# Kernel tuning notes

Hardware: AMD Instinct MI355X
Metric: run time of the kernel (lower is better)

Reference implementation:

```python
import jax, jax.numpy as jnp
import numpy as np

N = 20000      # nodes
E = 320000     # edges
F = 32         # node_feat_dim
H = 128        # hidden_dim
HEADS = 4
DH = 128       # out_channels per head (PyG TransformerConv semantics)
L = 2          # number of GNNBlocks actually built


def _ln(x, s, b, eps=1e-5):
    m = x.mean(-1, keepdims=True)
    v = ((x - m) ** 2).mean(-1, keepdims=True)
    return (x - m) / jnp.sqrt(v + eps) * s + b


def setup_inputs() -> dict:
    key = jax.random.key(0)
    ks = jax.random.split(key, 16)
    nrm = lambda k, sh, sc=0.05: jax.random.normal(k, sh, dtype=jnp.float32) * sc
    inp = {}
    inp['x'] = jax.random.normal(ks[0], (N, F), dtype=jnp.float32)
    inp['edge_index'] = jax.random.randint(ks[1], (2, E), 0, N)
    inp['Win'] = nrm(ks[2], (F, H))
    inp['b_in'] = jnp.zeros((H,), jnp.float32)
    inp['ln1_s'] = jnp.ones((L, H), jnp.float32)
    inp['ln1_b'] = jnp.zeros((L, H), jnp.float32)
    inp['Wq'] = nrm(ks[3], (L, H, HEADS * DH))
    inp['bq'] = jnp.zeros((L, HEADS * DH), jnp.float32)
    inp['Wk'] = nrm(ks[4], (L, H, HEADS * DH))
    inp['bk'] = jnp.zeros((L, HEADS * DH), jnp.float32)
    inp['Wv'] = nrm(ks[5], (L, H, HEADS * DH))
    inp['bv'] = jnp.zeros((L, HEADS * DH), jnp.float32)
    inp['Wskip'] = nrm(ks[6], (L, H, H))
    inp['bskip'] = jnp.zeros((L, H), jnp.float32)
    inp['Wbeta'] = nrm(ks[7], (L, 3 * H, 1))
    inp['ln2_s'] = jnp.ones((L, H), jnp.float32)
    inp['ln2_b'] = jnp.zeros((L, H), jnp.float32)
    inp['W1'] = nrm(ks[8], (L, H, 4 * H))
    inp['b1'] = jnp.zeros((L, 4 * H), jnp.float32)
    inp['W2'] = nrm(ks[9], (L, 4 * H, H))
    inp['b2'] = jnp.zeros((L, H), jnp.float32)
    inp['g1'] = jnp.ones((L,), jnp.float32)
    inp['g2'] = jnp.ones((L,), jnp.float32)
    inp['lno_s'] = jnp.ones((H,), jnp.float32)
    inp['lno_b'] = jnp.zeros((H,), jnp.float32)
    return inp


def reference(x, edge_index, Win, b_in, ln1_s, ln1_b, Wq, bq, Wk, bk, Wv, bv,
              Wskip, bskip, Wbeta, ln2_s, ln2_b, W1, b1, W2, b2, g1, g2,
              lno_s, lno_b):
    src, dst = edge_index[0], edge_index[1]  # messages flow src -> dst
    n = x.shape[0]
    scale = 1.0 / np.sqrt(DH).astype(np.float32)
    h = x @ Win + b_in  # [N,H]
    for l in range(L):
        # --- pre-norm TransformerConv (heads=4, concat=False, beta=True) ---
        hn = _ln(h, ln1_s[l], ln1_b[l])
        q = (hn @ Wq[l] + bq[l]).reshape(n, HEADS, DH)
        k = (hn @ Wk[l] + bk[l]).reshape(n, HEADS, DH)
        v = (hn @ Wv[l] + bv[l]).reshape(n, HEADS, DH)
        # per-edge attention logits [E, HEADS]
        alpha = jnp.einsum('ehd,ehd->eh', q[dst], k[src]) * scale
        # segment softmax over incoming edges of each target node
        amax = jax.ops.segment_max(alpha, dst, num_segments=n)  # [N,HEADS]
        num = jnp.exp(alpha - amax[dst])
        den = jax.ops.segment_sum(num, dst, num_segments=n)      # [N,HEADS]
        a = num / den[dst]                                       # [E,HEADS]
        # scatter-aggregate weighted values, then mean over heads (concat=False)
        agg = jax.ops.segment_sum(a[:, :, None] * v[src], dst, num_segments=n)
        out = agg.mean(axis=1)                                   # [N,H]
        # root skip + beta gate
        xr = hn @ Wskip[l] + bskip[l]
        beta = jax.nn.sigmoid(
            jnp.concatenate([out, xr, out - xr], axis=-1) @ Wbeta[l])  # [N,1]
        attn = beta * xr + (1.0 - beta) * out
        h = h + g1[l] * attn
        # --- pre-norm FFN ---
        hn2 = _ln(h, ln2_s[l], ln2_b[l])
        ffn = jax.nn.gelu(hn2 @ W1[l] + b1[l], approximate=False) @ W2[l] + b2[l]
        h = h + g2[l] * ffn
    return _ln(h, lno_s, lno_b)
```

## Files before the change

### kernel.cpp

```cpp
#include <hip/hip_runtime.h>
#include <hip/hip_bf16.h>
#include <math.h>

#define NN 20000
#define NE 320000

typedef unsigned short ushort_t;
typedef unsigned short ushortx8 __attribute__((ext_vector_type(8)));
typedef short s16x8 __attribute__((ext_vector_type(8)));
typedef float f32x4 __attribute__((ext_vector_type(4)));
typedef float f32x2 __attribute__((ext_vector_type(2)));

__device__ __forceinline__ float us2f(unsigned short u){
  return __uint_as_float(((unsigned)u) << 16);
}
__device__ __forceinline__ unsigned short f2us(float f){
  unsigned u = __float_as_uint(f);
  unsigned r = (u + 0x7fffu + ((u >> 16) & 1u)) >> 16;
  return (unsigned short)r;
}
__device__ __forceinline__ void e4m3x8_to_f32(uint2 d, float* out){
  f32x2 a = __builtin_amdgcn_cvt_pk_f32_fp8(d.x, false);
  f32x2 b = __builtin_amdgcn_cvt_pk_f32_fp8(d.x, true);
  f32x2 c = __builtin_amdgcn_cvt_pk_f32_fp8(d.y, false);
  f32x2 e = __builtin_amdgcn_cvt_pk_f32_fp8(d.y, true);
  out[0] = a.x; out[1] = a.y; out[2] = b.x; out[3] = b.y;
  out[4] = c.x; out[5] = c.y; out[6] = e.x; out[7] = e.y;
}
__device__ __forceinline__ uint2 f32x8_to_e4m3(const float* f){
  unsigned lo = __builtin_amdgcn_cvt_pk_fp8_f32(f[0], f[1], 0u, false);
  lo = __builtin_amdgcn_cvt_pk_fp8_f32(f[2], f[3], lo, true);
  unsigned hi = __builtin_amdgcn_cvt_pk_fp8_f32(f[4], f[5], 0u, false);
  hi = __builtin_amdgcn_cvt_pk_fp8_f32(f[6], f[7], hi, true);
  return make_uint2(lo, hi);
}
template<int CTRL>
__device__ __forceinline__ float dpp_add(float x){
  int t = __builtin_amdgcn_update_dpp(0, __float_as_int(x), CTRL, 0xf, 0xf, true);
  return x + __int_as_float(t);
}
__device__ __forceinline__ float red16(float p){
  p = dpp_add<0xB1>(p);
  p = dpp_add<0x4E>(p);
  p = dpp_add<0x141>(p);
  p = dpp_add<0x140>(p);
  return p;
}

__global__ void k_hist(const int* __restrict__ ei, int* __restrict__ deg){
  int e = blockIdx.x * 256 + threadIdx.x;
  if (e < NE) atomicAdd(&deg[ei[NE + e]], 1);
}

__global__ __launch_bounds__(1024) void k_scan(const int* __restrict__ deg,
                                               int* __restrict__ rowst,
                                               int* __restrict__ cur){
  __shared__ int ws[16];
  int tid = threadIdx.x;
  int lane = tid & 63, wid = tid >> 6;
  int base = tid * 20;
  int v[20];
  int s = 0;
  #pragma unroll
  for (int u = 0; u < 20; u++){
    int i = base + u;
    int d = (i < NN) ? deg[i] : 0;
    v[u] = s;
    s += d;
  }
  int incl = s;
  #pragma unroll
  for (int off = 1; off < 64; off <<= 1){
    int t = __shfl_up(incl, off);
    if (lane >= off) incl += t;
  }
  if (lane == 63) ws[wid] = incl;
  __syncthreads();
  int woff = 0;
  #pragma unroll
  for (int k2 = 0; k2 < 16; k2++) if (k2 < wid) woff += ws[k2];
  int toff = woff + incl - s;
  #pragma unroll
  for (int u = 0; u < 20; u++){
    int i = base + u;
    if (i < NN){ int e = toff + v[u]; rowst[i] = e; cur[i] = e; }
  }
  if (tid == 1023) rowst[NN] = toff + s;
}

__global__ void k_scatter(const int* __restrict__ ei, int* __restrict__ cur,
                          int* __restrict__ srcs){
  int e = blockIdx.x * 256 + threadIdx.x;
  if (e < NE){
    int s = ei[e];
    int d = ei[NE + e];
    int p = atomicAdd(&cur[d], 1);
    srcs[p] = s;
  }
}

__global__ void k_wt(const float* __restrict__ Wq, const float* __restrict__ Wk,
                     const float* __restrict__ Wv, const float* __restrict__ Wsk,
                     const float* __restrict__ W1, const float* __restrict__ W2,
                     const float* __restrict__ bq, const float* __restrict__ bk,
                     const float* __restrict__ bv, const float* __restrict__ bsk,
                     ushort_t* __restrict__ out, float* __restrict__ bcat,
                     int* __restrict__ deg){
  int f = blockIdx.x * 256 + threadIdx.x;
  if (f < 688128){
    float val;
    if (f < 425984){
      int l = f / 212992, idx = f % 212992;
      int n = idx / 128, kk = idx % 128;
      if (n < 512)       val = Wq[(size_t)l * 65536 + kk * 512 + n];
      else if (n < 1024) val = Wk[(size_t)l * 65536 + kk * 512 + (n - 512)];
      else if (n < 1536) val = Wv[(size_t)l * 65536 + kk * 512 + (n - 1024)];
      else               val = Wsk[(size_t)l * 16384 + kk * 128 + (n - 1536)];
    } else if (f < 557056){
      int idx = f - 425984;
      int l = idx / 65536, r = idx % 65536;
      int n = r / 128, kk = r % 128;
      val = W1[(size_t)l * 65536 + kk * 512 + n];
    } else {
      int idx = f - 557056;
      int l = idx / 65536, r = idx % 65536;
      int n = r / 512, kk = r % 512;
      val = W2[(size_t)l * 65536 + kk * 128 + n];
    }
    out[f] = f2us(val);
  } else if (f < 691456){
    int i = f - 688128;
    int l = i / 1664, c = i % 1664;
    float v;
    if (c < 512)       v = bq[l * 512 + c];
    else if (c < 1024) v = bk[l * 512 + c - 512];
    else if (c < 1536) v = bv[l * 512 + c - 1024];
    else               v = bsk[l * 128 + c - 1536];
    bcat[i] = v;
  } else if (f < 711456){
    deg[f - 691456] = 0;
  }
}

__global__ __launch_bounds__(128) void k_inproj(const float* __restrict__ x,
                                                const float* __restrict__ Win,
                                                const float* __restrict__ bin,
                                                float* __restrict__ h,
                                                const float* __restrict__ sc,
                                                const float* __restrict__ bi,
                                                ushort_t* __restrict__ hn){
  __shared__ float sW[32 * 128];
  __shared__ float sx[16][32];
  int tid = threadIdx.x;
  for (int i = 0; i < 32; i++) sW[i * 128 + tid] = Win[i * 128 + tid];
  int r0 = blockIdx.x * 16;
  for (int rr = tid >> 5; rr < 16; rr += 4){
    int gr = r0 + rr;
    sx[rr][tid & 31] = (gr < NN) ? x[(size_t)gr * 32 + (tid & 31)] : 0.f;
  }
  __syncthreads();
  float bias = bin[tid];
  for (int r = 0; r < 16; r++){
    int gr = r0 + r;
    if (gr >= NN) break;
    float acc = bias;
    #pragma unroll
    for (int k2 = 0; k2 < 32; k2++) acc += sx[r][k2] * sW[k2 * 128 + tid];
    h[(size_t)gr * 128 + tid] = acc;
  }
  __threadfence_block();
  __syncthreads();
  int lane = tid & 63, wv = tid >> 6;
  for (int rr = 0; rr < 8; rr++){
    int r = wv * 8 + rr;
    int gr = r0 + r;
    if (gr >= NN) continue;
    const float* p = h + (size_t)gr * 128 + lane * 2;
    float x0 = p[0], x1 = p[1];
    float sum = x0 + x1;
    for (int m = 1; m < 64; m <<= 1) sum += __shfl_xor(sum, m);
    float mean = sum * (1.f / 128.f);
    float d0 = x0 - mean, d1 = x1 - mean;
    float vs = d0 * d0 + d1 * d1;
    for (int m = 1; m < 64; m <<= 1) vs += __shfl_xor(vs, m);
    float rstd = rsqrtf(vs * (1.f / 128.f) + 1e-5f);
    int d = lane * 2;
    ushort_t* o = hn + (size_t)gr * 128 + d;
    o[0] = f2us(d0 * rstd * sc[d] + bi[d]);
    o[1] = f2us(d1 * rstd * sc[d + 1] + bi[d + 1]);
  }
}

template<int MODE>
__global__ __launch_bounds__(256) void k_mm(const ushort_t* __restrict__ A, int M, int K,
                                            const ushort_t* __restrict__ Bt,
                                            const float* __restrict__ bias,
                                            void* __restrict__ Cp, int ldc,
                                            const float* __restrict__ gptr,
                                            ushort_t* __restrict__ qout,
                                            unsigned char* __restrict__ kvout,
                                            ushort_t* __restrict__ xrout,
                                            int nbn,
                                            const float* __restrict__ lns,
                                            const float* __restrict__ lnb,
                                            void* __restrict__ lnout){
  __shared__ ushort_t smem[2 * 128 * 72];
  ushort_t* As = smem;
  ushort_t* Bs = smem + 128 * 72;
  int tid = threadIdx.x;
  int nwg = gridDim.x;
  int orig = blockIdx.x;
  int q8 = nwg >> 3, r8 = nwg & 7;
  int xcd = orig & 7, jj = orig >> 3;
  int wgid = (xcd < r8) ? (xcd * (q8 + 1) + jj)
                        : (r8 * (q8 + 1) + (xcd - r8) * q8 + jj);
  int m0 = (wgid / nbn) * 128, n0 = (wgid % nbn) * 128;
  int lane = tid & 63, w = tid >> 6;
  int wm = (w >> 1) * 64, wn = (w & 1) * 64;
  int fr = lane & 15, fq = lane >> 4;
  f32x4 acc[4][4];
  #pragma unroll
  for (int i = 0; i < 4; i++)
    #pragma unroll
    for (int j = 0; j < 4; j++) acc[i][j] = (f32x4){0.f, 0.f, 0.f, 0.f};

  for (int k0 = 0; k0 < K; k0 += 64){
    __syncthreads();
    #pragma unroll
    for (int it = 0; it < 4; it++){
      int idx = it * 256 + tid;
      int row = idx >> 3, ks = (idx & 7) * 8;
      int gr = m0 + row; if (gr >= M) gr = M - 1;
      *(ushortx8*)&As[row * 72 + ks] = *(const ushortx8*)(A + (size_t)gr * K + k0 + ks);
      *(ushortx8*)&Bs[row * 72 + ks] = *(const ushortx8*)(Bt + (size_t)(n0 + row) * K + k0 + ks);
    }
    __syncthreads();
    #pragma unroll
    for (int ks = 0; ks < 64; ks += 32){
      s16x8 a[4], b[4];
      #pragma unroll
      for (int i = 0; i < 4; i++)
        a[i] = *(const s16x8*)&As[(wm + i * 16 + fr) * 72 + ks + fq * 8];
      #pragma unroll
      for (int j = 0; j < 4; j++)
        b[j] = *(const s16x8*)&Bs[(wn + j * 16 + fr) * 72 + ks + fq * 8];
      #pragma unroll
      for (int i = 0; i < 4; i++)
        #pragma unroll
        for (int j = 0; j < 4; j++)
          acc[i][j] = __builtin_amdgcn_mfma_f32_16x16x32_bf16(a[i], b[j], acc[i][j], 0, 0, 0);
    }
  }

  if (MODE == 2 || MODE == 5){
    float g = *gptr;
    #pragma unroll
    for (int i = 0; i < 4; i++){
      int grb = m0 + wm + i * 16 + fq * 4;
      #pragma unroll
      for (int r = 0; r < 4; r++){
        int gr = grb + r;
        if (gr >= M) continue;
        #pragma unroll
        for (int j = 0; j < 4; j++){
          int gc = n0 + wn + j * 16 + fr;
          float c = acc[i][j][r] + bias[gc];
          float* hp = (float*)Cp + (size_t)gr * ldc + gc;
          *hp = *hp + g * c;
        }
      }
    }
    __threadfence_block();
    __syncthreads();
    int w4 = tid >> 6;
    for (int rr = 0; rr < 32; rr++){
      int row = w4 * 32 + rr;
      int gr = m0 + row;
      if (gr >= M) continue;
      const float* p = (const float*)Cp + (size_t)gr * ldc + lane * 2;
      float x0 = p[0], x1 = p[1];
      float sum = x0 + x1;
      for (int m = 1; m < 64; m <<= 1) sum += __shfl_xor(sum, m);
      float mean = sum * (1.f / 128.f);
      float d0 = x0 - mean, d1 = x1 - mean;
      float vs = d0 * d0 + d1 * d1;
      for (int m = 1; m < 64; m <<= 1) vs += __shfl_xor(vs, m);
      float rstd = rsqrtf(vs * (1.f / 128.f) + 1e-5f);
      int d = lane * 2;
      float o0 = d0 * rstd * lns[d] + lnb[d];
      float o1 = d1 * rstd * lns[d + 1] + lnb[d + 1];
      if (MODE == 2){
        ushort_t* o = (ushort_t*)lnout + (size_t)gr * 128 + d;
        o[0] = f2us(o0); o[1] = f2us(o1);
      } else {
        float* o = (float*)lnout + (size_t)gr * 128 + d;
        o[0] = o0; o[1] = o1;
      }
    }
    return;
  }

  __syncthreads();
  ushort_t* Cs = smem;
  #pragma unroll
  for (int i = 0; i < 4; i++){
    int rowb = wm + i * 16 + fq * 4;
    #pragma unroll
    for (int j = 0; j < 4; j++){
      int col = wn + j * 16 + fr;
      float bv = bias[n0 + col];
      #pragma unroll
      for (int r = 0; r < 4; r++){
        float c = acc[i][j][r] + bv;
        if (MODE == 1) c = 0.5f * c * (1.f + erff(c * 0.70710678118654752f));
        Cs[(rowb + r) * 136 + col] = f2us(c);
      }
    }
  }
  __syncthreads();
  #pragma unroll
  for (int it = 0; it < 8; it++){
    int idx = it * 256 + tid;
    int row = idx >> 4, seg = idx & 15;
    int gr = m0 + row;
    if (gr >= M) continue;
    ushortx8 cv = *(const ushortx8*)&Cs[row * 136 + seg * 8];
    int gc = n0 + seg * 8;
    if (MODE == 1){
      *(ushortx8*)((ushort_t*)Cp + (size_t)gr * ldc + gc) = cv;
    } else {
      if (n0 < 512){
        *(ushortx8*)(qout + (size_t)gr * 512 + gc) = cv;
      } else if (n0 < 1536){
        float fv[8];
        #pragma unroll
        for (int t = 0; t < 8; t++) fv[t] = us2f(cv[t]);
        uint2 pk = f32x8_to_e4m3(fv);
        if (n0 < 1024){
          *(uint2*)(kvout + (size_t)gr * 1024 + (size_t)((gc - 512) >> 3) * 16) = pk;
        } else {
          *(uint2*)(kvout + (size_t)gr * 1024 + (size_t)((gc - 1024) >> 3) * 16 + 8) = pk;
        }
      } else {
        *(ushortx8*)(xrout + (size_t)gr * 128 + (gc - 1536)) = cv;
      }
    }
  }
}

#define EDGE_PROC(KVD) {                                                     \
    float kf[8]; e4m3x8_to_f32(make_uint2((KVD).x, (KVD).y), kf);            \
    float p = 0.f;                                                           \
    _Pragma("unroll")                                                        \
    for (int t = 0; t < 8; t++) p += qf[t] * kf[t];                          \
    p = red16(p);                                                            \
    float wgt = __expf(p * scale);                                           \
    float vf[8]; e4m3x8_to_f32(make_uint2((KVD).z, (KVD).w), vf);            \
    l += wgt;                                                                \
    _Pragma("unroll")                                                        \
    for (int t = 0; t < 8; t++) acc[t] += wgt * vf[t];                       \
  }

__global__ void k_attn(const ushort_t* __restrict__ q, const unsigned char* __restrict__ kv8,
                       const int* __restrict__ rowst, const int* __restrict__ srcs,
                       const ushort_t* __restrict__ xr, const float* __restrict__ Wb,
                       const float* __restrict__ g1p, float* __restrict__ h,
                       const float* __restrict__ sc2, const float* __restrict__ bi2,
                       ushort_t* __restrict__ hn){
  int n = blockIdx.x * 4 + (threadIdx.x >> 6);
  int lane = threadIdx.x & 63;
  if (n >= NN) return;
  int s0 = rowst[n], s1 = rowst[n + 1];
  int deg = s1 - s0;
  float qf[8];
  {
    ushortx8 qv = *((const ushortx8*)(q + (size_t)n * 512) + lane);
    #pragma unroll
    for (int t = 0; t < 8; t++) qf[t] = us2f(qv[t]);
  }
  const float scale = 0.08838834764831845f;
  const uint4* kvb = (const uint4*)kv8;
  float l = 0.f;
  float acc[8] = {0.f, 0.f, 0.f, 0.f, 0.f, 0.f, 0.f, 0.f};
  for (int c0 = s0; c0 < s1; c0 += 64){
    int rem = s1 - c0; if (rem > 64) rem = 64;
    int se = (lane < rem) ? srcs[c0 + lane] : 0;
    uint4 bufA[8], bufB[8];
    int jA = 0;
    int cA = rem < 8 ? rem : 8;
    #pragma unroll
    for (int u = 0; u < 8; u++)
      if (u < cA)
        bufA[u] = kvb[(size_t)__builtin_amdgcn_readlane(se, u) * 64 + lane];
    while (jA < rem){
      int jB = jA + cA;
      int cB = rem - jB; cB = cB < 0 ? 0 : (cB > 8 ? 8 : cB);
      #pragma unroll
      for (int u = 0; u < 8; u++)
        if (u < cB)
          bufB[u] = kvb[(size_t)__builtin_amdgcn_readlane(se, jB + u) * 64 + lane];
      #pragma unroll
      for (int u = 0; u < 8; u++)
        if (u < cA) EDGE_PROC(bufA[u]);
      int jA2 = jB + cB;
      int cA2 = rem - jA2; cA2 = cA2 < 0 ? 0 : (cA2 > 8 ? 8 : cA2);
      #pragma unroll
      for (int u = 0; u < 8; u++)
        if (u < cA2)
          bufA[u] = kvb[(size_t)__builtin_amdgcn_readlane(se, jA2 + u) * 64 + lane];
      #pragma unroll
      for (int u = 0; u < 8; u++)
        if (u < cB) EDGE_PROC(bufB[u]);
      jA = jA2; cA = cA2;
    }
  }
  float inv = deg ? (0.25f / l) : 0.f;
  #pragma unroll
  for (int t = 0; t < 8; t++){
    float r = acc[t] * inv;
    r += __shfl_xor(r, 16); r += __shfl_xor(r, 32);
    acc[t] = r;
  }
  if (lane < 16){
    int d = lane * 8;
    float xv[8];
    {
      ushortx8 xrv = *(const ushortx8*)(xr + (size_t)n * 128 + d);
      #pragma unroll
      for (int t = 0; t < 8; t++) xv[t] = us2f(xrv[t]);
    }
    float pp = 0.f;
    #pragma unroll
    for (int t = 0; t < 8; t++){
      float w0 = Wb[d + t], w1 = Wb[128 + d + t], w2 = Wb[256 + d + t];
      pp += acc[t] * (w0 + w2) + xv[t] * (w1 - w2);
    }
    pp = red16(pp);
    float beta = 1.f / (1.f + __expf(-pp));
    float g = *g1p;
    float* hp = h + (size_t)n * 128 + d;
    float hv[8];
    {
      float4 h0 = *(const float4*)(hp);
      float4 h1 = *(const float4*)(hp + 4);
      hv[0]=h0.x; hv[1]=h0.y; hv[2]=h0.z; hv[3]=h0.w;
      hv[4]=h1.x; hv[5]=h1.y; hv[6]=h1.z; hv[7]=h1.w;
    }
    #pragma unroll
    for (int t = 0; t < 8; t++)
      hv[t] += g * (beta * xv[t] + (1.f - beta) * acc[t]);
    float s = 0.f;
    #pragma unroll
    for (int t = 0; t < 8; t++) s += hv[t];
    s = red16(s);
    float mean = s * (1.f / 128.f);
    float vs = 0.f;
    #pragma unroll
    for (int t = 0; t < 8; t++){ float dd = hv[t] - mean; vs += dd * dd; }
    vs = red16(vs);
    float rstd = rsqrtf(vs * (1.f / 128.f) + 1e-5f);
    *(float4*)(hp) = make_float4(hv[0], hv[1], hv[2], hv[3]);
    *(float4*)(hp + 4) = make_float4(hv[4], hv[5], hv[6], hv[7]);
    ushortx8 hno;
    #pragma unroll
    for (int t = 0; t < 8; t++)
      hno[t] = f2us((hv[t] - mean) * rstd * sc2[d + t] + bi2[d + t]);
    *(ushortx8*)(hn + (size_t)n * 128 + d) = hno;
  }
}

extern "C" void kernel_launch(void* const* d_in, const int* in_sizes, int n_in,
                              void* d_out, int out_size, void* d_ws, size_t ws_size,
                              hipStream_t stream){
  const float* x    = (const float*)d_in[0];
  const int*   ei   = (const int*)d_in[1];
  const float* Win  = (const float*)d_in[2];
  const float* bin  = (const float*)d_in[3];
  const float* ln1s = (const float*)d_in[4];
  const float* ln1b = (const float*)d_in[5];
  const float* Wq   = (const float*)d_in[6];
  const float* bq   = (const float*)d_in[7];
  const float* Wk   = (const float*)d_in[8];
  const float* bk   = (const float*)d_in[9];
  const float* Wv   = (const float*)d_in[10];
  const float* bv   = (const float*)d_in[11];
  const float* Wsk  = (const float*)d_in[12];
  const float* bsk  = (const float*)d_in[13];
  const float* Wbt  = (const float*)d_in[14];
  const float* ln2s = (const float*)d_in[15];
  const float* ln2b = (const float*)d_in[16];
  const float* W1   = (const float*)d_in[17];
  const float* b1   = (const float*)d_in[18];
  const float* W2   = (const float*)d_in[19];
  const float* b2   = (const float*)d_in[20];
  const float* g1   = (const float*)d_in[21];
  const float* g2   = (const float*)d_in[22];
  const float* lnos = (const float*)d_in[23];
  const float* lnob = (const float*)d_in[24];

  char* wsb = (char*)d_ws;
  size_t off = 0;
  float*         h    = (float*)(wsb + off);         off += (size_t)NN * 128 * 4;
  ushort_t*      hn   = (ushort_t*)(wsb + off);      off += (size_t)NN * 128 * 2;
  ushort_t*      qbuf = (ushort_t*)(wsb + off);      off += (size_t)NN * 512 * 2;
  unsigned char* kv8  = (unsigned char*)(wsb + off); off += (size_t)NN * 1024;
  ushort_t*      xrb  = (ushort_t*)(wsb + off);      off += (size_t)NN * 128 * 2;
  ushort_t*      tb   = (ushort_t*)(wsb + off);      off += (size_t)NN * 512 * 2;
  ushort_t*      wt   = (ushort_t*)(wsb + off);      off += (size_t)688128 * 2;
  float*         bcat = (float*)(wsb + off);         off += (size_t)3328 * 4;
  int*           deg   = (int*)(wsb + off);          off += (size_t)NN * 4;
  int*           rowst = (int*)(wsb + off);          off += (size_t)(NN + 4) * 4;
  int*           cur   = (int*)(wsb + off);          off += (size_t)NN * 4;
  int*           srcs  = (int*)(wsb + off);          off += (size_t)NE * 4;
  ushort_t* Wcat = wt;
  ushort_t* W1t  = wt + 425984;
  ushort_t* W2t  = wt + 557056;

  k_wt<<<2780, 256, 0, stream>>>(Wq, Wk, Wv, Wsk, W1, W2, bq, bk, bv, bsk, wt, bcat, deg);
  k_hist<<<(NE + 255) / 256, 256, 0, stream>>>(ei, deg);
  k_scan<<<1, 1024, 0, stream>>>(deg, rowst, cur);
  k_scatter<<<(NE + 255) / 256, 256, 0, stream>>>(ei, cur, srcs);
  k_inproj<<<NN / 16, 128, 0, stream>>>(x, Win, bin, h, ln1s, ln1b, hn);

  for (int l = 0; l < 2; l++){
    k_mm<3><<<157 * 13, 256, 0, stream>>>(hn, NN, 128, Wcat + (size_t)l * 212992, bcat + l * 1664,
                                          nullptr, 0, nullptr, qbuf, kv8, xrb, 13,
                                          nullptr, nullptr, nullptr);
    k_attn<<<(NN + 3) / 4, 256, 0, stream>>>(qbuf, kv8, rowst, srcs, xrb, Wbt + l * 384,
                                             g1 + l, h, ln2s + l * 128, ln2b + l * 128, hn);
    k_mm<1><<<157 * 4, 256, 0, stream>>>(hn, NN, 128, W1t + (size_t)l * 65536, b1 + l * 512,
                                         tb, 512, nullptr, nullptr, nullptr, nullptr, 4,
                                         nullptr, nullptr, nullptr);
    if (l == 0){
      k_mm<2><<<157, 256, 0, stream>>>(tb, NN, 512, W2t, b2, h, 128, g2,
                                       nullptr, nullptr, nullptr, 1,
                                       ln1s + 128, ln1b + 128, hn);
    } else {
      k_mm<5><<<157, 256, 0, stream>>>(tb, NN, 512, W2t + 65536, b2 + 128, h, 128, g2 + 1,
                                       nullptr, nullptr, nullptr, 1,
                                       lnos, lnob, d_out);
    }
  }
}
```

Baseline: 497.0 us.

## Unfuse LayerNorm from W2 GEMM and simplify attention gather batching

Moves the LayerNorm that followed the W2 GEMM epilogue out into a standalone row-parallel k_ln kernel, launched before the second layer's QKV GEMM and after the final layer. This removes the serial per-block 32-row LN loop and the block-level fence and barrier from the GEMM. The cost is two extra launches and another read of h. The attention kernel's double-buffered 8-edge K/V gather pipeline is also replaced with simple batches of 12, then 4, then single edges, which trades explicit load/compute overlap for more loads in flight per batch.

```diff
diff --git a/kernel.cpp b/kernel.cpp
--- a/kernel.cpp
+++ b/kernel.cpp
@@ -191,6 +191,33 @@
   }
 }
 
+template<int OUTBF16>
+__global__ void k_ln(const float* __restrict__ in, const float* __restrict__ sc,
+                     const float* __restrict__ bi, void* __restrict__ outp, int rows){
+  int row = blockIdx.x * 4 + (threadIdx.x >> 6);
+  int lane = threadIdx.x & 63;
+  if (row >= rows) return;
+  const float* p = in + (size_t)row * 128 + lane * 2;
+  float x0 = p[0], x1 = p[1];
+  float sum = x0 + x1;
+  for (int m = 1; m < 64; m <<= 1) sum += __shfl_xor(sum, m);
+  float mean = sum * (1.f / 128.f);
+  float d0 = x0 - mean, d1 = x1 - mean;
+  float vs = d0 * d0 + d1 * d1;
+  for (int m = 1; m < 64; m <<= 1) vs += __shfl_xor(vs, m);
+  float rstd = rsqrtf(vs * (1.f / 128.f) + 1e-5f);
+  int d = lane * 2;
+  float o0 = d0 * rstd * sc[d] + bi[d];
+  float o1 = d1 * rstd * sc[d + 1] + bi[d + 1];
+  if (OUTBF16){
+    ushort_t* o = (ushort_t*)outp + (size_t)row * 128 + d;
+    o[0] = f2us(o0); o[1] = f2us(o1);
+  } else {
+    float* o = (float*)outp + (size_t)row * 128 + d;
+    o[0] = o0; o[1] = o1;
+  }
+}
+
 template<int MODE>
 __global__ __launch_bounds__(256) void k_mm(const ushort_t* __restrict__ A, int M, int K,
                                             const ushort_t* __restrict__ Bt,
@@ -200,10 +227,7 @@
                                             ushort_t* __restrict__ qout,
                                             unsigned char* __restrict__ kvout,
                                             ushort_t* __restrict__ xrout,
-                                            int nbn,
-                                            const float* __restrict__ lns,
-                                            const float* __restrict__ lnb,
-                                            void* __restrict__ lnout){
+                                            int nbn){
   __shared__ ushort_t smem[2 * 128 * 72];
   ushort_t* As = smem;
   ushort_t* Bs = smem + 128 * 72;
@@ -252,7 +276,7 @@
     }
   }
 
-  if (MODE == 2 || MODE == 5){
+  if (MODE == 2){
     float g = *gptr;
     #pragma unroll
     for (int i = 0; i < 4; i++){
@@ -265,36 +289,8 @@
         for (int j = 0; j < 4; j++){
           int gc = n0 + wn + j * 16 + fr;
           float c = acc[i][j][r] + bias[gc];
-          float* hp = (float*)Cp + (size_t)gr * ldc + gc;
-          *hp = *hp + g * c;
+          ((float*)Cp)[(size_t)gr * ldc + gc] += g * c;
         }
-      }
-    }
-    __threadfence_block();
-    __syncthreads();
-    int w4 = tid >> 6;
-    for (int rr = 0; rr < 32; rr++){
-      int row = w4 * 32 + rr;
-      int gr = m0 + row;
-      if (gr >= M) continue;
-      const float* p = (const float*)Cp + (size_t)gr * ldc + lane * 2;
-      float x0 = p[0], x1 = p[1];
-      float sum = x0 + x1;
-      for (int m = 1; m < 64; m <<= 1) sum += __shfl_xor(sum, m);
-      float mean = sum * (1.f / 128.f);
-      float d0 = x0 - mean, d1 = x1 - mean;
-      float vs = d0 * d0 + d1 * d1;
-      for (int m = 1; m < 64; m <<= 1) vs += __shfl_xor(vs, m);
-      float rstd = rsqrtf(vs * (1.f / 128.f) + 1e-5f);
-      int d = lane * 2;
-      float o0 = d0 * rstd * lns[d] + lnb[d];
-      float o1 = d1 * rstd * lns[d + 1] + lnb[d + 1];
-      if (MODE == 2){
-        ushort_t* o = (ushort_t*)lnout + (size_t)gr * 128 + d;
-        o[0] = f2us(o0); o[1] = f2us(o1);
-      } else {
-        float* o = (float*)lnout + (size_t)gr * 128 + d;
-        o[0] = o0; o[1] = o1;
       }
     }
     return;
@@ -385,33 +381,31 @@
   for (int c0 = s0; c0 < s1; c0 += 64){
     int rem = s1 - c0; if (rem > 64) rem = 64;
     int se = (lane < rem) ? srcs[c0 + lane] : 0;
-    uint4 bufA[8], bufB[8];
-    int jA = 0;
-    int cA = rem < 8 ? rem : 8;
-    #pragma unroll
-    for (int u = 0; u < 8; u++)
-      if (u < cA)
-        bufA[u] = kvb[(size_t)__builtin_amdgcn_readlane(se, u) * 64 + lane];
-    while (jA < rem){
-      int jB = jA + cA;
-      int cB = rem - jB; cB = cB < 0 ? 0 : (cB > 8 ? 8 : cB);
-      #pragma unroll
-      for (int u = 0; u < 8; u++)
-        if (u < cB)
-          bufB[u] = kvb[(size_t)__builtin_amdgcn_readlane(se, jB + u) * 64 + lane];
-      #pragma unroll
-      for (int u = 0; u < 8; u++)
-        if (u < cA) EDGE_PROC(bufA[u]);
-      int jA2 = jB + cB;
-      int cA2 = rem - jA2; cA2 = cA2 < 0 ? 0 : (cA2 > 8 ? 8 : cA2);
-      #pragma unroll
-      for (int u = 0; u < 8; u++)
-        if (u < cA2)
-          bufA[u] = kvb[(size_t)__builtin_amdgcn_readlane(se, jA2 + u) * 64 + lane];
-      #pragma unroll
-      for (int u = 0; u < 8; u++)
-        if (u < cB) EDGE_PROC(bufB[u]);
-      jA = jA2; cA = cA2;
+    int j = 0;
+    for (; j + 12 <= rem; j += 12){
+      uint4 kvd[12];
+      #pragma unroll
+      for (int u = 0; u < 12; u++){
+        int sv = __builtin_amdgcn_readlane(se, j + u);
+        kvd[u] = kvb[(size_t)sv * 64 + lane];
+      }
+      #pragma unroll
+      for (int u = 0; u < 12; u++) EDGE_PROC(kvd[u]);
+    }
+    for (; j + 4 <= rem; j += 4){
+      uint4 kvd[4];
+      #pragma unroll
+      for (int u = 0; u < 4; u++){
+        int sv = __builtin_amdgcn_readlane(se, j + u);
+        kvd[u] = kvb[(size_t)sv * 64 + lane];
+      }
+      #pragma unroll
+      for (int u = 0; u < 4; u++) EDGE_PROC(kvd[u]);
+    }
+    for (; j < rem; j++){
+      int sv0 = __builtin_amdgcn_readlane(se, j);
+      uint4 kvd = kvb[(size_t)sv0 * 64 + lane];
+      EDGE_PROC(kvd);
     }
   }
   float inv = deg ? (0.25f / l) : 0.f;
@@ -523,22 +517,16 @@
   k_inproj<<<NN / 16, 128, 0, stream>>>(x, Win, bin, h, ln1s, ln1b, hn);
 
   for (int l = 0; l < 2; l++){
+    if (l == 1)
+      k_ln<1><<<(NN + 3) / 4, 256, 0, stream>>>(h, ln1s + 128, ln1b + 128, hn, NN);
     k_mm<3><<<157 * 13, 256, 0, stream>>>(hn, NN, 128, Wcat + (size_t)l * 212992, bcat + l * 1664,
-                                          nullptr, 0, nullptr, qbuf, kv8, xrb, 13,
-                                          nullptr, nullptr, nullptr);
+                                          nullptr, 0, nullptr, qbuf, kv8, xrb, 13);
     k_attn<<<(NN + 3) / 4, 256, 0, stream>>>(qbuf, kv8, rowst, srcs, xrb, Wbt + l * 384,
                                              g1 + l, h, ln2s + l * 128, ln2b + l * 128, hn);
     k_mm<1><<<157 * 4, 256, 0, stream>>>(hn, NN, 128, W1t + (size_t)l * 65536, b1 + l * 512,
-                                         tb, 512, nullptr, nullptr, nullptr, nullptr, 4,
-                                         nullptr, nullptr, nullptr);
-    if (l == 0){
-      k_mm<2><<<157, 256, 0, stream>>>(tb, NN, 512, W2t, b2, h, 128, g2,
-                                       nullptr, nullptr, nullptr, 1,
-                                       ln1s + 128, ln1b + 128, hn);
-    } else {
-      k_mm<5><<<157, 256, 0, stream>>>(tb, NN, 512, W2t + 65536, b2 + 128, h, 128, g2 + 1,
-                                       nullptr, nullptr, nullptr, 1,
-                                       lnos, lnob, d_out);
-    }
-  }
-}
+                                         tb, 512, nullptr, nullptr, nullptr, nullptr, 4);
+    k_mm<2><<<157, 256, 0, stream>>>(tb, NN, 512, W2t + (size_t)l * 65536, b2 + l * 128,
+                                     h, 128, g2 + l, nullptr, nullptr, nullptr, 1);
+  }
+  k_ln<0><<<(NN + 3) / 4, 256, 0, stream>>>(h, lnos, lnob, (float*)d_out, NN);
+}
```

Result: faster. 431.0 us (-13.3%).
